# Performance work log

Measured on AMD Instinct MI355X. Metric: run time of the kernel, lower is better.

The kernel has to match this reference:

```python
import jax, jax.numpy as jnp
import numpy as np
import math

D_MODEL = 1024
EXPAND = 2
D_INNER = D_MODEL * EXPAND          # 2048
D_STATE = 16
NHEADS = 8
NGROUPS = 1
D_CONV = 4
HEADDIM = D_INNER // NHEADS         # 256
CONV_DIM = D_INNER + 2 * NGROUPS * D_STATE   # x, B, C go through the causal conv
D_IN_PROJ = 2 * D_INNER + 2 * NGROUPS * D_STATE + NHEADS  # z, xBC, dt
CHUNK = 64
BATCH = 4
SEQLEN = 4096


def setup_inputs() -> dict:
    key = jax.random.key(0)
    ks = jax.random.split(key, 6)
    rng = np.random.default_rng(0)
    u = jax.random.normal(ks[0], (BATCH, SEQLEN, D_MODEL), dtype=jnp.float32)
    W_in = jax.random.normal(ks[1], (D_MODEL, D_IN_PROJ), dtype=jnp.float32) * 0.02
    conv_w = jax.random.normal(ks[2], (CONV_DIM, D_CONV), dtype=jnp.float32) * (1.0 / math.sqrt(D_CONV))
    conv_b = jnp.zeros((CONV_DIM,), dtype=jnp.float32)
    # dt_bias = inverse-softplus of dt sampled log-uniform in [dt_min, dt_max]
    dt = np.exp(rng.uniform(size=NHEADS) * (math.log(0.1) - math.log(0.001)) + math.log(0.001))
    dt = np.clip(dt, 1e-4, None)
    dt_bias = jnp.asarray(dt + np.log(-np.expm1(-dt)), dtype=jnp.float32)
    # A in A_init_range=(0.9, 0.999), stored as A_log with A = -exp(A_log)
    A_log = jnp.asarray(np.log(rng.uniform(0.9, 0.999, NHEADS)), dtype=jnp.float32)
    D = jnp.ones((NHEADS,), dtype=jnp.float32)
    norm_w = jnp.ones((D_INNER,), dtype=jnp.float32)
    W_out = jax.random.normal(ks[3], (D_INNER, D_MODEL), dtype=jnp.float32) * 0.02
    return {"u": u, "W_in": W_in, "conv_w": conv_w, "conv_b": conv_b,
            "dt_bias": dt_bias, "A_log": A_log, "D": D, "norm_w": norm_w, "W_out": W_out}


def _mamba2_fwd(u, W_in, conv_w, conv_b, dt_bias, A_log, D, norm_w, W_out):
    b, l, _ = u.shape
    h, p, n, g, Q = NHEADS, HEADDIM, D_STATE, NGROUPS, CHUNK
    zxbcdt = u @ W_in                                   # [b,l,2*d_inner+2gn+h]
    z = zxbcdt[..., :D_INNER]
    xBC = zxbcdt[..., D_INNER:D_INNER + CONV_DIM]
    dt = jax.nn.softplus(zxbcdt[..., D_INNER + CONV_DIM:] + dt_bias)  # [b,l,h]
    # causal depthwise conv over time (d_conv taps) + SiLU
    xp = jnp.pad(xBC, ((0, 0), (D_CONV - 1, 0), (0, 0)))
    xconv = conv_b
    for k in range(D_CONV):
        xconv = xconv + xp[:, k:k + l, :] * conv_w[:, k]
    xBC = jax.nn.silu(xconv)
    x = xBC[..., :D_INNER].reshape(b, l, h, p)
    B = xBC[..., D_INNER:D_INNER + g * n].reshape(b, l, g, n)
    C = xBC[..., D_INNER + g * n:].reshape(b, l, g, n)
    Bh = jnp.repeat(B, h // g, axis=2)                  # [b,l,h,n]
    Ch = jnp.repeat(C, h // g, axis=2)
    A = -jnp.exp(A_log)                                 # [h]
    # ---- chunked (SSD) selective scan ----
    nc = l // Q
    xc = x.reshape(b, nc, Q, h, p)
    dtc = dt.reshape(b, nc, Q, h)
    Bc = Bh.reshape(b, nc, Q, h, n)
    Cc = Ch.reshape(b, nc, Q, h, n)
    a = dtc * A                                         # [b,nc,Q,h]
    cs = jnp.cumsum(a, axis=2).transpose(0, 1, 3, 2)    # [b,nc,h,Q]
    mask = jnp.tril(jnp.ones((Q, Q), dtype=bool))
    L = jnp.where(mask, jnp.exp(cs[..., :, None] - cs[..., None, :]), 0.0)  # [b,nc,h,Q,Q]
    xdt = xc * dtc[..., None]                           # x scaled by dt
    Y_diag = jnp.einsum('bcqhn,bcshn,bchqs,bcshp->bcqhp', Cc, Bc, L, xdt)
    decay_states = jnp.exp(cs[..., -1:] - cs)           # [b,nc,h,Q]
    states = jnp.einsum('bcqhn,bchq,bcqhp->bchpn', Bc, decay_states, xdt)  # per-chunk state
    chunk_decay = jnp.exp(cs[..., -1])                  # [b,nc,h]
    def step(carry, inp):
        st, dec = inp
        new = dec[..., None, None] * carry + st
        return new, carry
    init = jnp.zeros((b, h, p, n), dtype=u.dtype)
    _, prev = jax.lax.scan(step, init, (states.transpose(1, 0, 2, 3, 4), chunk_decay.transpose(1, 0, 2)))
    prev = prev.transpose(1, 0, 2, 3, 4)                # state entering each chunk [b,nc,h,p,n]
    Y_off = jnp.einsum('bcqhn,bchpn,bchq->bcqhp', Cc, prev, jnp.exp(cs))
    y = (Y_diag + Y_off).reshape(b, l, h, p) + D[:, None] * x
    y = y.reshape(b, l, D_INNER)
    # gated RMSNorm then out projection
    y = y * jax.nn.silu(z)
    y = y * jax.lax.rsqrt(jnp.mean(y * y, axis=-1, keepdims=True) + 1e-5) * norm_w
    return y @ W_out


def reference(u, W_in, conv_w, conv_b, dt_bias, A_log, D, norm_w, W_out):
    return _mamba2_fwd(u, W_in, conv_w, conv_b, dt_bias, A_log, D, norm_w, W_out)
```

## Files before the change

kernel.cpp:

```cpp
#include <hip/hip_runtime.h>
#include <cstddef>
#include <cstdint>
#include <type_traits>

constexpr int DM = 1024;
constexpr int DI = 2048;
constexpr int DS = 16;
constexpr int NH = 8;
constexpr int CD = 2080;
constexpr int DP = 4136;
constexpr int DPT = 4224;
constexpr int Q  = 64;
constexpr int B_ = 4;
constexpr int L_ = 4096;
constexpr int NCH = 64;
constexpr int HP = 256;
constexpr int NR = B_ * L_;

constexpr size_t AL(size_t x) { return (x + 255) & ~(size_t)255; }
constexpr size_t OFFB_ZX = 0;
constexpr size_t OFFB_BC = AL(OFFB_ZX + (size_t)NR * DP * 2);
constexpr size_t OFFB_DT = AL(OFFB_BC + (size_t)NR * 32 * 4);
constexpr size_t OFFB_CS = AL(OFFB_DT + (size_t)NR * NH * 4);
constexpr size_t OFFB_ST = AL(OFFB_CS + (size_t)B_ * NCH * NH * Q * 4);
constexpr size_t OFFB_Y  = AL(OFFB_ST + (size_t)B_ * NCH * NH * HP * DS * 4);
constexpr size_t OFFB_WO = AL(OFFB_Y + (size_t)NR * DI * 2);

__device__ __forceinline__ float silu_f(float x) { return x / (1.f + expf(-x)); }
__device__ __forceinline__ float bf2f(unsigned short v) {
  unsigned int u = ((unsigned int)v) << 16;
  return __builtin_bit_cast(float, u);
}
__device__ __forceinline__ unsigned short f2bf(float f) {
  unsigned int u = __builtin_bit_cast(unsigned int, f);
  u += 0x7FFFu + ((u >> 16) & 1u);
  return (unsigned short)(u >> 16);
}

typedef __attribute__((ext_vector_type(8))) short bf16x8;
typedef __attribute__((ext_vector_type(4))) float f32x4;

template<bool OUT_BF16>
__global__ __launch_bounds__(256)
void gemm_mfma(const unsigned short* __restrict__ A, const unsigned short* __restrict__ Bt,
               void* __restrict__ Cout, int M, int N, int K, int ldc) {
  __shared__ unsigned short As[128 * 64];
  __shared__ unsigned short Bs[128 * 64];
  const int t = threadIdx.x;
  const int w = t >> 6, l = t & 63;
  const int quad = l >> 4, lan = l & 15;
  const int wm = w >> 1, wn = w & 1;
  const int row0 = blockIdx.y * 128, col0 = blockIdx.x * 128;

  f32x4 acc[4][4];
  #pragma unroll
  for (int i = 0; i < 4; ++i)
    #pragma unroll
    for (int j = 0; j < 4; ++j)
      acc[i][j] = (f32x4)(0.0f);

  for (int k0 = 0; k0 < K; k0 += 64) {
    __syncthreads();
    #pragma unroll
    for (int i = 0; i < 4; ++i) {
      const int jc = i * 256 + w * 64 + l;
      const int m = jc >> 3, c8 = jc & 7;
      const int gc8 = c8 ^ (m & 7);
      const unsigned short* gp = A + (size_t)(row0 + m) * K + k0 + (gc8 << 3);
      unsigned short* lp = &As[(size_t)(i * 256 + w * 64) * 8];
      __builtin_amdgcn_global_load_lds((const __attribute__((address_space(1))) void*)gp,
                                       (__attribute__((address_space(3))) void*)lp, 16, 0, 0);
    }
    #pragma unroll
    for (int i = 0; i < 4; ++i) {
      const int jc = i * 256 + w * 64 + l;
      const int n = jc >> 3, c8 = jc & 7;
      const int gc8 = c8 ^ (n & 7);
      const unsigned short* gp = Bt + (size_t)(col0 + n) * K + k0 + (gc8 << 3);
      unsigned short* lp = &Bs[(size_t)(i * 256 + w * 64) * 8];
      __builtin_amdgcn_global_load_lds((const __attribute__((address_space(1))) void*)gp,
                                       (__attribute__((address_space(3))) void*)lp, 16, 0, 0);
    }
    __syncthreads();
    #pragma unroll
    for (int kk = 0; kk < 64; kk += 32) {
      const int kc = quad + (kk >> 3);
      bf16x8 af[4], bf[4];
      #pragma unroll
      for (int mi = 0; mi < 4; ++mi) {
        const int m = wm * 64 + mi * 16 + lan;
        af[mi] = *(const bf16x8*)&As[m * 64 + ((kc ^ (m & 7)) << 3)];
      }
      #pragma unroll
      for (int ni = 0; ni < 4; ++ni) {
        const int n = wn * 64 + ni * 16 + lan;
        bf[ni] = *(const bf16x8*)&Bs[n * 64 + ((kc ^ (n & 7)) << 3)];
      }
      #pragma unroll
      for (int mi = 0; mi < 4; ++mi)
        #pragma unroll
        for (int ni = 0; ni < 4; ++ni)
          acc[mi][ni] = __builtin_amdgcn_mfma_f32_16x16x32_bf16(af[mi], bf[ni], acc[mi][ni], 0, 0, 0);
    }
  }
  #pragma unroll
  for (int mi = 0; mi < 4; ++mi) {
    const size_t rb = row0 + wm * 64 + mi * 16 + quad * 4;
    #pragma unroll
    for (int ni = 0; ni < 4; ++ni) {
      const int colb = col0 + wn * 64 + ni * 16 + lan;
      if (colb < N) {
        if constexpr (OUT_BF16) {
          unsigned short* C = (unsigned short*)Cout;
          #pragma unroll
          for (int r = 0; r < 4; ++r)
            C[(rb + r) * (size_t)ldc + colb] = f2bf(acc[mi][ni][r]);
        } else {
          float* C = (float*)Cout;
          #pragma unroll
          for (int r = 0; r < 4; ++r)
            C[(rb + r) * (size_t)ldc + colb] = acc[mi][ni][r];
        }
      }
    }
  }
}

__global__ __launch_bounds__(256)
void cvt_bf16(const float* __restrict__ src, unsigned short* __restrict__ dst, size_t n4) {
  const size_t i = ((size_t)blockIdx.x * 256 + threadIdx.x) * 4;
  if (i < n4 * 4) {
    float4 v = *(const float4*)(src + i);
    ushort4 o;
    o.x = f2bf(v.x); o.y = f2bf(v.y); o.z = f2bf(v.z); o.w = f2bf(v.w);
    *(ushort4*)(dst + i) = o;
  }
}

__global__ __launch_bounds__(256)
void transpose_cvt(const float* __restrict__ src, unsigned short* __restrict__ dst,
                   int R, int C, int Cvalid) {
  __shared__ float T[64][65];
  const int t = threadIdx.x;
  const int n0 = blockIdx.x * 64, k0 = blockIdx.y * 64;
  #pragma unroll
  for (int i = 0; i < 4; ++i) {
    int f = t + i * 256;
    int r = f >> 4, c4 = (f & 15) << 2;
    int n = n0 + c4;
    float4 v = make_float4(0.f, 0.f, 0.f, 0.f);
    if (n + 3 < Cvalid) {
      v = *(const float4*)(src + (size_t)(k0 + r) * C + n);
    } else {
      if (n + 0 < Cvalid) v.x = src[(size_t)(k0 + r) * C + n + 0];
      if (n + 1 < Cvalid) v.y = src[(size_t)(k0 + r) * C + n + 1];
      if (n + 2 < Cvalid) v.z = src[(size_t)(k0 + r) * C + n + 2];
      if (n + 3 < Cvalid) v.w = src[(size_t)(k0 + r) * C + n + 3];
    }
    T[r][c4 + 0] = v.x; T[r][c4 + 1] = v.y; T[r][c4 + 2] = v.z; T[r][c4 + 3] = v.w;
  }
  __syncthreads();
  #pragma unroll
  for (int i = 0; i < 4; ++i) {
    int f = t + i * 256;
    int c = f >> 4, r4 = (f & 15) << 2;
    ushort4 o;
    o.x = f2bf(T[r4 + 0][c]); o.y = f2bf(T[r4 + 1][c]);
    o.z = f2bf(T[r4 + 2][c]); o.w = f2bf(T[r4 + 3][c]);
    *(ushort4*)(dst + (size_t)(n0 + c) * R + k0 + r4) = o;
  }
}

__global__ __launch_bounds__(256)
void convbc_kernel(const unsigned short* __restrict__ zx, const float* __restrict__ cw,
                   const float* __restrict__ cb, float* __restrict__ bc) {
  const int idx = blockIdx.x * 256 + threadIdx.x;
  const int j = idx & 31;
  const int row = idx >> 5;
  const int l = row & (L_ - 1);
  const int cc = DI + j;
  float a = cb[cc];
  #pragma unroll
  for (int k = 0; k < 4; ++k) {
    int ll = l - 3 + k;
    if (ll >= 0)
      a += bf2f(zx[(size_t)(row - 3 + k) * DP + (DI + DI + j)]) * cw[cc * 4 + k];
  }
  bc[(size_t)row * 32 + j] = silu_f(a);
}

__global__ __launch_bounds__(256)
void dt_kernel(const unsigned short* __restrict__ zx, const float* __restrict__ dt_bias,
               float* __restrict__ dt) {
  const int i = blockIdx.x * 256 + threadIdx.x;
  const int h = i & 7;
  const size_t row = (size_t)(i >> 3);
  float x = bf2f(zx[row * DP + (DI + CD) + h]) + dt_bias[h];
  dt[i] = (x > 20.f) ? x : log1pf(expf(x));
}

__global__ __launch_bounds__(256)
void chunk_kernel(const unsigned short* __restrict__ zx, const float* __restrict__ bc,
                  const float* __restrict__ dt, const float* __restrict__ A_log,
                  const float* __restrict__ cw, const float* __restrict__ cb,
                  const float* __restrict__ Dp, float* __restrict__ cs_out,
                  float* __restrict__ states, unsigned short* __restrict__ yb) {
  const int c = blockIdx.x, h = blockIdx.y, b = blockIdx.z;
  const int t = threadIdx.x;
  const int w = t >> 6, l = t & 63;
  const int quad = l >> 4, lan = l & 15;
  __shared__ float dtS[Q], csS[Q], ddS[Q];
  __shared__ float BsS[Q][DS + 1];
  __shared__ float CsS[Q][DS];
  __shared__ __align__(16) unsigned short Msd[Q][Q + 8];
  __shared__ __align__(16) unsigned short BdT[DS][Q + 8];
  __shared__ __align__(16) unsigned short xsT[Q][Q + 8];
  __shared__ __align__(16) unsigned short rawS[Q + 3][Q];
  const size_t rowb = (size_t)b * L_ + (size_t)c * Q;

  if (t < Q) dtS[t] = dt[(rowb + t) * NH + h];
  __syncthreads();
  if (t == 0) {
    float A = -expf(A_log[h]);
    float s = 0.f;
    for (int q = 0; q < Q; ++q) { s += dtS[q] * A; csS[q] = s; }
  }
  __syncthreads();
  if (t < Q) {
    ddS[t] = expf(csS[Q - 1] - csS[t]) * dtS[t];
    cs_out[(((size_t)b * NCH + c) * NH + h) * Q + t] = csS[t];
  }
  for (int i = t; i < Q * DS; i += 256) {
    int q = i >> 4, n = i & 15;
    BsS[q][n] = bc[(rowb + q) * 32 + n];
    CsS[q][n] = bc[(rowb + q) * 32 + 16 + n];
  }
  __syncthreads();
  for (int i = t; i < DS * Q; i += 256) {
    int n = i & 15, q = i >> 4;
    BdT[n][q] = f2bf(BsS[q][n] * ddS[q]);
  }
  const float Dh = Dp[h];
  for (int i = t; i < Q * Q; i += 256) {
    int q = i >> 6, s = i & 63;
    float v = 0.f;
    if (s <= q) {
      float d = 0.f;
      #pragma unroll
      for (int n = 0; n < DS; ++n) d += CsS[q][n] * BsS[s][n];
      v = expf(csS[q] - csS[s]) * d * dtS[s];
      if (s == q) v += Dh;
    }
    Msd[q][s] = f2bf(v);
  }

  const int pch = t & 63, qb0 = t >> 6;

  for (int pt = 0; pt < 4; ++pt) {
    const int col0 = DI + h * HP + pt * Q;
    for (int v = t; v < 67 * 8; v += 256) {
      int i = v >> 3, p0 = (v & 7) * 8;
      int lg = c * Q - 3 + i;
      uint4 val = make_uint4(0, 0, 0, 0);
      if (lg >= 0)
        val = *(const uint4*)(zx + ((size_t)b * L_ + lg) * DP + col0 + p0);
      *(uint4*)&rawS[i][p0] = val;
    }
    __syncthreads();
    {
      const int cc = h * HP + pt * Q + pch;
      const float w0 = cw[cc * 4 + 0], w1 = cw[cc * 4 + 1];
      const float w2 = cw[cc * 4 + 2], w3 = cw[cc * 4 + 3];
      const float bias = cb[cc];
      #pragma unroll
      for (int i2 = 0; i2 < 16; ++i2) {
        int q = qb0 + 4 * i2;
        float a = bias + bf2f(rawS[q][pch]) * w0 + bf2f(rawS[q + 1][pch]) * w1
                       + bf2f(rawS[q + 2][pch]) * w2 + bf2f(rawS[q + 3][pch]) * w3;
        xsT[pch][q] = f2bf(silu_f(a));
      }
    }
    __syncthreads();
    bf16x8 xfrag[2];
    #pragma unroll
    for (int ks = 0; ks < 2; ++ks)
      xfrag[ks] = *(const bf16x8*)&xsT[w * 16 + lan][quad * 8 + ks * 32];
    {
      f32x4 sacc = (f32x4)(0.0f);
      #pragma unroll
      for (int ks = 0; ks < 2; ++ks) {
        bf16x8 bfr = *(const bf16x8*)&BdT[lan][quad * 8 + ks * 32];
        sacc = __builtin_amdgcn_mfma_f32_16x16x32_bf16(xfrag[ks], bfr, sacc, 0, 0, 0);
      }
      const int p = w * 16 + quad * 4;
      const size_t sb = ((((size_t)b * NCH + c) * NH + h) * HP + pt * Q + p) * DS + lan;
      #pragma unroll
      for (int r = 0; r < 4; ++r)
        states[sb + (size_t)r * DS] = sacc[r];
    }
    {
      #pragma unroll
      for (int mi = 0; mi < 4; ++mi) {
        f32x4 yac = (f32x4)(0.0f);
        #pragma unroll
        for (int ks = 0; ks < 2; ++ks) {
          bf16x8 am = *(const bf16x8*)&Msd[mi * 16 + lan][quad * 8 + ks * 32];
          yac = __builtin_amdgcn_mfma_f32_16x16x32_bf16(am, xfrag[ks], yac, 0, 0, 0);
        }
        const int qrow = mi * 16 + quad * 4;
        const int pcol = h * HP + pt * Q + w * 16 + lan;
        #pragma unroll
        for (int r = 0; r < 4; ++r)
          yb[(rowb + qrow + r) * (size_t)DI + pcol] = f2bf(yac[r]);
      }
    }
    __syncthreads();
  }
}

__global__ __launch_bounds__(256)
void scan_kernel(float* __restrict__ states, const float* __restrict__ cs) {
  const int pn = blockIdx.x * 256 + threadIdx.x;
  const int h = blockIdx.y, b = blockIdx.z;
  const size_t cstride = (size_t)NH * HP * DS;
  const size_t base = ((size_t)b * NCH * NH + h) * (size_t)(HP * DS) + pn;
  float carry = 0.f;
  for (int c = 0; c < NCH; ++c) {
    float dec = expf(cs[(((size_t)b * NCH + c) * NH + h) * Q + (Q - 1)]);
    float st = states[base + (size_t)c * cstride];
    states[base + (size_t)c * cstride] = carry;
    carry = dec * carry + st;
  }
}

__global__ __launch_bounds__(256)
void yoff_kernel(const float* __restrict__ bc, const float* __restrict__ cs,
                 const float* __restrict__ prev, unsigned short* __restrict__ yb) {
  const int c = blockIdx.x, h = blockIdx.y, b = blockIdx.z;
  const int t = threadIdx.x;
  __shared__ __align__(16) float CsS[Q][DS];
  __shared__ float ecs[Q];
  const size_t rowb = (size_t)b * L_ + (size_t)c * Q;
  const size_t pb = (((size_t)b * NCH + c) * NH + h) * (size_t)(HP * DS);
  for (int i = t; i < Q * DS; i += 256) {
    int q = i >> 4, n = i & 15;
    CsS[q][n] = bc[(rowb + q) * 32 + 16 + n];
  }
  if (t < Q) ecs[t] = expf(cs[(((size_t)b * NCH + c) * NH + h) * Q + t]);
  float pv[16];
  #pragma unroll
  for (int k = 0; k < 4; ++k)
    *(float4*)&pv[k * 4] = *(const float4*)(prev + pb + (size_t)t * DS + k * 4);
  __syncthreads();
  for (int q = 0; q < Q; ++q) {
    float acc = 0.f;
    #pragma unroll
    for (int n = 0; n < DS; ++n) acc += CsS[q][n] * pv[n];
    const size_t idx = (rowb + q) * DI + h * HP + t;
    yb[idx] = f2bf(bf2f(yb[idx]) + ecs[q] * acc);
  }
}

__global__ __launch_bounds__(256)
void gatenorm_kernel(const unsigned short* __restrict__ zx, const float* __restrict__ norm_w,
                     unsigned short* __restrict__ yb) {
  const size_t row = blockIdx.x;
  const int t = threadIdx.x;
  const unsigned short* zrow = zx + row * DP;
  unsigned short* yrow = yb + row * DI;
  const int d0 = t * 8;
  uint4 yv = *(const uint4*)(yrow + d0);
  uint4 zv = *(const uint4*)(zrow + d0);
  const unsigned short* ys = (const unsigned short*)&yv;
  const unsigned short* zs = (const unsigned short*)&zv;
  float v[8];
  float ss = 0.f;
  #pragma unroll
  for (int j = 0; j < 8; ++j) {
    float val = bf2f(ys[j]) * silu_f(bf2f(zs[j]));
    v[j] = val;
    ss += val * val;
  }
  #pragma unroll
  for (int off = 32; off > 0; off >>= 1) ss += __shfl_down(ss, off);
  __shared__ float red[4];
  if ((t & 63) == 0) red[t >> 6] = ss;
  __syncthreads();
  float tot = red[0] + red[1] + red[2] + red[3];
  float scale = rsqrtf(tot / (float)DI + 1e-5f);
  ushort4 o[2];
  unsigned short* op = (unsigned short*)o;
  #pragma unroll
  for (int j = 0; j < 8; ++j) op[j] = f2bf(v[j] * scale * norm_w[d0 + j]);
  *(uint4*)(yrow + d0) = *(uint4*)o;
}

extern "C" void kernel_launch(void* const* d_in, const int* in_sizes, int n_in,
                              void* d_out, int out_size, void* d_ws, size_t ws_size,
                              hipStream_t stream) {
  const float* u       = (const float*)d_in[0];
  const float* W_in    = (const float*)d_in[1];
  const float* conv_w  = (const float*)d_in[2];
  const float* conv_b  = (const float*)d_in[3];
  const float* dt_bias = (const float*)d_in[4];
  const float* A_log   = (const float*)d_in[5];
  const float* Dp      = (const float*)d_in[6];
  const float* norm_w  = (const float*)d_in[7];
  const float* W_out   = (const float*)d_in[8];
  float* out = (float*)d_out;
  char* w = (char*)d_ws;

  unsigned short* zx  = (unsigned short*)(w + OFFB_ZX);
  float* bcb          = (float*)(w + OFFB_BC);
  float* dtb          = (float*)(w + OFFB_DT);
  float* csb          = (float*)(w + OFFB_CS);
  float* stb          = (float*)(w + OFFB_ST);
  unsigned short* yb  = (unsigned short*)(w + OFFB_Y);
  unsigned short* ub  = (unsigned short*)(w + OFFB_ST);
  unsigned short* wib = (unsigned short*)(w + OFFB_Y);
  unsigned short* wob = (unsigned short*)(w + OFFB_WO);

  cvt_bf16<<<(NR * DM / 4 + 255) / 256, 256, 0, stream>>>(u, ub, (size_t)NR * DM / 4);
  transpose_cvt<<<dim3(DPT / 64, DM / 64), 256, 0, stream>>>(W_in, wib, DM, DP, DP);
  transpose_cvt<<<dim3(DM / 64, DI / 64), 256, 0, stream>>>(W_out, wob, DI, DM, DM);
  gemm_mfma<true><<<dim3(DPT / 128, NR / 128), 256, 0, stream>>>(
      ub, wib, zx, NR, DP, DM, DP);
  convbc_kernel<<<(NR * 32) / 256, 256, 0, stream>>>(zx, conv_w, conv_b, bcb);
  dt_kernel<<<(NR * NH) / 256, 256, 0, stream>>>(zx, dt_bias, dtb);
  chunk_kernel<<<dim3(NCH, NH, B_), 256, 0, stream>>>(zx, bcb, dtb, A_log, conv_w,
                                                      conv_b, Dp, csb, stb, yb);
  scan_kernel<<<dim3((HP * DS) / 256, NH, B_), 256, 0, stream>>>(stb, csb);
  yoff_kernel<<<dim3(NCH, NH, B_), 256, 0, stream>>>(bcb, csb, stb, yb);
  gatenorm_kernel<<<NR, 256, 0, stream>>>(zx, norm_w, yb);
  gemm_mfma<false><<<dim3(DM / 128, NR / 128), 256, 0, stream>>>(
      yb, wob, out, NR, DM, DI, DM);
}
```

Baseline: 578.8 us.

## Swizzle GEMM blocks per XCD and restructure chunk kernel loads and stores

The GEMM block index is remapped so that consecutive row tiles land on the same XCD, aiming for better L2 reuse of shared operands. In the chunk kernel, the serial cumulative sum is replaced by a wavefront shuffle scan. Raw conv inputs are prefetched into registers for the next tile while the current one is computed. Conv outputs are written as vectorised stores. State and y outputs are staged in reused shared memory and written back with coalesced 16-byte stores, which costs an extra barrier per tile.

```diff
diff --git a/kernel.cpp b/kernel.cpp
--- a/kernel.cpp
+++ b/kernel.cpp
@@ -50,7 +50,13 @@
   const int w = t >> 6, l = t & 63;
   const int quad = l >> 4, lan = l & 15;
   const int wm = w >> 1, wn = w & 1;
-  const int row0 = blockIdx.y * 128, col0 = blockIdx.x * 128;
+  const int ncol = gridDim.x;
+  const int id = blockIdx.y * ncol + blockIdx.x;
+  const int xcd = id & 7, slot = id >> 3;
+  const int rpx = gridDim.y >> 3;
+  const int row_g = xcd * rpx + slot / ncol;
+  const int col_g = slot - (slot / ncol) * ncol;
+  const int row0 = row_g * 128, col0 = col_g * 128;
 
   f32x4 acc[4][4];
   #pragma unroll
@@ -211,24 +217,30 @@
   const int quad = l >> 4, lan = l & 15;
   __shared__ float dtS[Q], csS[Q], ddS[Q];
   __shared__ float BsS[Q][DS + 1];
-  __shared__ float CsS[Q][DS];
   __shared__ __align__(16) unsigned short Msd[Q][Q + 8];
   __shared__ __align__(16) unsigned short BdT[DS][Q + 8];
-  __shared__ __align__(16) unsigned short xsT[Q][Q + 8];
-  __shared__ __align__(16) unsigned short rawS[Q + 3][Q];
+  __shared__ __align__(16) char regionA[Q * (Q + 8) * 2];
+  __shared__ __align__(16) char regionB[Q * DS * 4 + Q * (Q + 8) * 2];
+  float (*CsS)[DS]                 = (float(*)[DS])regionA;
+  unsigned short (*xsT)[Q + 8]     = (unsigned short(*)[Q + 8])regionA;
+  unsigned short (*rawS)[Q]        = (unsigned short(*)[Q])regionB;
+  float (*stS)[DS]                 = (float(*)[DS])regionB;
+  unsigned short (*ytS)[Q + 8]     = (unsigned short(*)[Q + 8])(regionB + Q * DS * 4);
   const size_t rowb = (size_t)b * L_ + (size_t)c * Q;
 
-  if (t < Q) dtS[t] = dt[(rowb + t) * NH + h];
-  __syncthreads();
-  if (t == 0) {
-    float A = -expf(A_log[h]);
-    float s = 0.f;
-    for (int q = 0; q < Q; ++q) { s += dtS[q] * A; csS[q] = s; }
-  }
-  __syncthreads();
   if (t < Q) {
-    ddS[t] = expf(csS[Q - 1] - csS[t]) * dtS[t];
-    cs_out[(((size_t)b * NCH + c) * NH + h) * Q + t] = csS[t];
+    float dtv = dt[(rowb + t) * NH + h];
+    dtS[t] = dtv;
+    float s = dtv * (-expf(A_log[h]));
+    #pragma unroll
+    for (int off = 1; off < 64; off <<= 1) {
+      float n = __shfl_up(s, off, 64);
+      if (t >= off) s += n;
+    }
+    csS[t] = s;
+    float slast = __shfl(s, 63, 64);
+    ddS[t] = expf(slast - s) * dtv;
+    cs_out[(((size_t)b * NCH + c) * NH + h) * Q + t] = s;
   }
   for (int i = t; i < Q * DS; i += 256) {
     int q = i >> 4, n = i & 15;
@@ -254,31 +266,45 @@
     Msd[q][s] = f2bf(v);
   }
 
-  const int pch = t & 63, qb0 = t >> 6;
+  const int pch = l;
+  uint4 r0 = make_uint4(0, 0, 0, 0), r1 = make_uint4(0, 0, 0, 0), r2 = make_uint4(0, 0, 0, 0);
+  {
+    const int col0 = DI + h * HP;
+    const unsigned short* gb = zx + ((size_t)b * L_ + (c * Q - 3)) * DP + col0;
+    if (c > 0 || t >= 24) r0 = *(const uint4*)(gb + (size_t)(t >> 3) * DP + (t & 7) * 8);
+    r1 = *(const uint4*)(gb + (size_t)((t + 256) >> 3) * DP + (t & 7) * 8);
+    if (t < 24) r2 = *(const uint4*)(gb + (size_t)((t + 512) >> 3) * DP + (t & 7) * 8);
+  }
 
   for (int pt = 0; pt < 4; ++pt) {
-    const int col0 = DI + h * HP + pt * Q;
-    for (int v = t; v < 67 * 8; v += 256) {
-      int i = v >> 3, p0 = (v & 7) * 8;
-      int lg = c * Q - 3 + i;
-      uint4 val = make_uint4(0, 0, 0, 0);
-      if (lg >= 0)
-        val = *(const uint4*)(zx + ((size_t)b * L_ + lg) * DP + col0 + p0);
-      *(uint4*)&rawS[i][p0] = val;
-    }
+    uint4* rw = (uint4*)rawS;
+    rw[t] = r0; rw[t + 256] = r1;
+    if (t < 24) rw[t + 512] = r2;
     __syncthreads();
     {
       const int cc = h * HP + pt * Q + pch;
       const float w0 = cw[cc * 4 + 0], w1 = cw[cc * 4 + 1];
       const float w2 = cw[cc * 4 + 2], w3 = cw[cc * 4 + 3];
       const float bias = cb[cc];
+      const int q0 = w * 16;
+      unsigned short ob[16];
       #pragma unroll
       for (int i2 = 0; i2 < 16; ++i2) {
-        int q = qb0 + 4 * i2;
+        int q = q0 + i2;
         float a = bias + bf2f(rawS[q][pch]) * w0 + bf2f(rawS[q + 1][pch]) * w1
                        + bf2f(rawS[q + 2][pch]) * w2 + bf2f(rawS[q + 3][pch]) * w3;
-        xsT[pch][q] = f2bf(silu_f(a));
-      }
+        ob[i2] = f2bf(silu_f(a));
+      }
+      *(uint4*)&xsT[pch][q0 + 0] = *(uint4*)&ob[0];
+      *(uint4*)&xsT[pch][q0 + 8] = *(uint4*)&ob[8];
+    }
+    if (pt < 3) {
+      const int col0n = DI + h * HP + (pt + 1) * Q;
+      const unsigned short* gb = zx + ((size_t)b * L_ + (c * Q - 3)) * DP + col0n;
+      r0 = make_uint4(0, 0, 0, 0); r2 = make_uint4(0, 0, 0, 0);
+      if (c > 0 || t >= 24) r0 = *(const uint4*)(gb + (size_t)(t >> 3) * DP + (t & 7) * 8);
+      r1 = *(const uint4*)(gb + (size_t)((t + 256) >> 3) * DP + (t & 7) * 8);
+      if (t < 24) r2 = *(const uint4*)(gb + (size_t)((t + 512) >> 3) * DP + (t & 7) * 8);
     }
     __syncthreads();
     bf16x8 xfrag[2];
@@ -292,11 +318,9 @@
         bf16x8 bfr = *(const bf16x8*)&BdT[lan][quad * 8 + ks * 32];
         sacc = __builtin_amdgcn_mfma_f32_16x16x32_bf16(xfrag[ks], bfr, sacc, 0, 0, 0);
       }
-      const int p = w * 16 + quad * 4;
-      const size_t sb = ((((size_t)b * NCH + c) * NH + h) * HP + pt * Q + p) * DS + lan;
       #pragma unroll
       for (int r = 0; r < 4; ++r)
-        states[sb + (size_t)r * DS] = sacc[r];
+        stS[w * 16 + quad * 4 + r][lan] = sacc[r];
     }
     {
       #pragma unroll
@@ -307,11 +331,22 @@
           bf16x8 am = *(const bf16x8*)&Msd[mi * 16 + lan][quad * 8 + ks * 32];
           yac = __builtin_amdgcn_mfma_f32_16x16x32_bf16(am, xfrag[ks], yac, 0, 0, 0);
         }
-        const int qrow = mi * 16 + quad * 4;
-        const int pcol = h * HP + pt * Q + w * 16 + lan;
         #pragma unroll
         for (int r = 0; r < 4; ++r)
-          yb[(rowb + qrow + r) * (size_t)DI + pcol] = f2bf(yac[r]);
+          ytS[mi * 16 + quad * 4 + r][w * 16 + lan] = f2bf(yac[r]);
+      }
+    }
+    __syncthreads();
+    {
+      const size_t stbase = ((((size_t)b * NCH + c) * NH + h) * HP + (size_t)pt * Q) * DS;
+      ((float4*)(states + stbase))[t] = ((const float4*)&stS[0][0])[t];
+    }
+    {
+      const int colbase = h * HP + pt * Q;
+      #pragma unroll
+      for (int pass = 0; pass < 2; ++pass) {
+        int q = pass * 32 + (t >> 3), p8 = (t & 7) * 8;
+        *(uint4*)(yb + (rowb + q) * (size_t)DI + colbase + p8) = *(const uint4*)&ytS[q][p8];
       }
     }
     __syncthreads();
```

Measured after the change: 549.0 us. 5.2% less time.
